# Optimization experiments

Hardware: AMD Instinct MI355X
Metric: run time of the kernel (lower is better)

The kernel has to match this reference:

```python
import jax, jax.numpy as jnp
import numpy as np

H = 512
L = 4096
LOC_CNT = 100000


def setup_inputs() -> dict:
    key = jax.random.key(0)
    ks = jax.random.split(key, 12)
    stdv = 1.0 / np.sqrt(H)

    def unif(k, shape):
        return jax.random.uniform(k, shape, dtype=jnp.float32, minval=-stdv, maxval=stdv)

    return {
        "td_upper": jax.random.uniform(ks[0], (L,), dtype=jnp.float32),
        "td_lower": jax.random.uniform(ks[1], (L,), dtype=jnp.float32),
        "ld_upper": jax.random.uniform(ks[2], (L,), dtype=jnp.float32),
        "ld_lower": jax.random.uniform(ks[3], (L,), dtype=jnp.float32),
        "loc": jax.random.randint(ks[4], (L,), 0, LOC_CNT, dtype=jnp.int64),
        "hx": jax.random.normal(ks[5], (H, 1), dtype=jnp.float32),
        "W_ih": unif(ks[6], (H, H)),
        "W_th_upper": unif(ks[7], (H, H)),
        "W_th_lower": unif(ks[8], (H, H)),
        "W_sh_upper": unif(ks[9], (H, H)),
        "W_sh_lower": unif(ks[10], (H, H)),
        "loc_table": unif(ks[11], (LOC_CNT, H)),
    }


def reference(td_upper, td_lower, ld_upper, ld_lower, loc, hx,
              W_ih, W_th_upper, W_th_lower, W_sh_upper, W_sh_lower, loc_table):
    # Gather location embeddings: (L, H)
    emb = loc_table[loc]
    # Ttd[i] @ emb[i] where Ttd[i] = (W_tu*tu_i + W_tl*tl_i)/(tu_i+tl_i):
    # distribute the scalar-weighted combine over the matmul.
    a = emb @ W_th_upper.T            # (L, H) == (W_th_upper @ emb[i])^T per row
    b = emb @ W_th_lower.T
    v = (a * td_upper[:, None] + b * td_lower[:, None]) / (td_upper + td_lower)[:, None]
    # Sld[i] @ v[i]
    c = v @ W_sh_upper.T
    d = v @ W_sh_lower.T
    w = (c * ld_upper[:, None] + d * ld_lower[:, None]) / (ld_upper + ld_lower)[:, None]
    # Original: torch.sum(torch.cat(...)) -> full scalar reduction over all L*H values.
    loc_vec = jnp.sum(w)
    usr_vec = W_ih @ hx               # (H, 1)
    return jax.nn.sigmoid(loc_vec + usr_vec)
```

## Files before the change

### kernel.cpp

```cpp
#include <hip/hip_runtime.h>
#include <math.h>

namespace {

constexpr int H = 512;
constexpr int L = 4096;
constexpr int REPG = 8;
constexpr int REPS = 4;

constexpr int WS_SU  = 0;
constexpr int WS_SL  = WS_SU + REPS * H;
constexpr int WS_G   = WS_SL + REPS * H;
constexpr int WS_IHV = WS_G + REPG * 4 * H;
constexpr int WS_ACC = WS_IHV + H;
constexpr int WS_CNT = WS_ACC + 1;
constexpr int WS_TOT = WS_CNT + 1;

constexpr int GB = 128;
constexpr int CB = 128;
constexpr int WB = 8;
constexpr int BGRID = 128;

__device__ inline float wave_reduce(float v) {
#pragma unroll
    for (int off = 32; off; off >>= 1) v += __shfl_xor(v, off, 64);
    return v;
}

__global__ __launch_bounds__(512) void stageA_k(
    const float* __restrict__ tu, const float* __restrict__ tl,
    const float* __restrict__ lu, const float* __restrict__ ll,
    const int* __restrict__ loc, const float* __restrict__ table,
    const float* __restrict__ Wsu, const float* __restrict__ Wsl,
    const float* __restrict__ Wih, const float* __restrict__ hx,
    float* __restrict__ ws) {
    const int b = blockIdx.x;
    const int t = threadIdx.x;
    if (b < GB) {
        const int rep = b & (REPG - 1);
        float aa = 0.f, ab = 0.f, ag = 0.f, ad = 0.f;
        const int row0 = b * (L / GB);
#pragma unroll 16
        for (int r = 0; r < L / GB; ++r) {
            const int row = row0 + r;
            const float tuv = tu[row], tlv = tl[row];
            const float luv = lu[row], llv = ll[row];
            const float ti = 1.f / (tuv + tlv), li = 1.f / (luv + llv);
            const float Tu = tuv * ti, Tl = tlv * ti;
            const float Lu = luv * li, Ll = llv * li;
            const float e = table[(size_t)loc[row] * H + t];
            aa += Lu * Tu * e;
            ab += Lu * Tl * e;
            ag += Ll * Tu * e;
            ad += Ll * Tl * e;
        }
        float* g = ws + WS_G + rep * (4 * H);
        atomicAdd(g + 0 * H + t, aa);
        atomicAdd(g + 1 * H + t, ab);
        atomicAdd(g + 2 * H + t, ag);
        atomicAdd(g + 3 * H + t, ad);
    } else if (b < GB + CB) {
        const int cb = b - GB;
        const int mat = cb >> 6;
        const int q = cb & 63;
        const int m0 = q * (H / 64);
        const int rep = q & (REPS - 1);
        const float* W = mat ? Wsl : Wsu;
        float acc = 0.f;
#pragma unroll
        for (int r = 0; r < H / 64; ++r) acc += W[(size_t)(m0 + r) * H + t];
        atomicAdd(ws + (mat ? WS_SL : WS_SU) + rep * H + t, acc);
    } else {
        const int wb = b - GB - CB;
        const int lane = t & 63, wid = t >> 6;
        const int j = lane * 8;
        const float4 xA = *reinterpret_cast<const float4*>(hx + j);
        const float4 xB = *reinterpret_cast<const float4*>(hx + j + 4);
#pragma unroll
        for (int r = 0; r < 8; ++r) {
            const int row = wb * 64 + wid * 8 + r;
            const float4 wA = *reinterpret_cast<const float4*>(Wih + (size_t)row * H + j);
            const float4 wB = *reinterpret_cast<const float4*>(Wih + (size_t)row * H + j + 4);
            float a = wA.x * xA.x + wA.y * xA.y + wA.z * xA.z + wA.w * xA.w
                    + wB.x * xB.x + wB.y * xB.y + wB.z * xB.z + wB.w * xB.w;
            a = wave_reduce(a);
            if (lane == 0) ws[WS_IHV + row] = a;
        }
    }
}

__global__ __launch_bounds__(512) void stageB_k(
    const float* __restrict__ Wtu, const float* __restrict__ Wtl,
    float* __restrict__ ws, float* __restrict__ out) {
    const int t = threadIdx.x;
    const int lane = t & 63, wid = t >> 6;
    const int gw = blockIdx.x * 8 + wid;
    const int mat = gw >> 9;
    const int h = gw & (H - 1);
    const float* W = mat ? Wtl : Wtu;
    const int v1 = mat ? 1 : 0;
    const int v2 = mat ? 3 : 2;

    float suh = 0.f, slh = 0.f;
#pragma unroll
    for (int rp = 0; rp < REPS; ++rp) {
        suh += ws[WS_SU + rp * H + h];
        slh += ws[WS_SL + rp * H + h];
    }

    const int j = lane * 8;
    float a1[8] = {0, 0, 0, 0, 0, 0, 0, 0};
    float a2[8] = {0, 0, 0, 0, 0, 0, 0, 0};
#pragma unroll
    for (int rp = 0; rp < REPG; ++rp) {
        const float* g1 = ws + WS_G + (rp * 4 + v1) * H + j;
        const float* g2 = ws + WS_G + (rp * 4 + v2) * H + j;
        const float4 x0 = *reinterpret_cast<const float4*>(g1);
        const float4 x1 = *reinterpret_cast<const float4*>(g1 + 4);
        const float4 y0 = *reinterpret_cast<const float4*>(g2);
        const float4 y1 = *reinterpret_cast<const float4*>(g2 + 4);
        a1[0] += x0.x; a1[1] += x0.y; a1[2] += x0.z; a1[3] += x0.w;
        a1[4] += x1.x; a1[5] += x1.y; a1[6] += x1.z; a1[7] += x1.w;
        a2[0] += y0.x; a2[1] += y0.y; a2[2] += y0.z; a2[3] += y0.w;
        a2[4] += y1.x; a2[5] += y1.y; a2[6] += y1.z; a2[7] += y1.w;
    }

    const float4 wA = *reinterpret_cast<const float4*>(W + (size_t)h * H + j);
    const float4 wB = *reinterpret_cast<const float4*>(W + (size_t)h * H + j + 4);
    float acc = wA.x * (suh * a1[0] + slh * a2[0])
              + wA.y * (suh * a1[1] + slh * a2[1])
              + wA.z * (suh * a1[2] + slh * a2[2])
              + wA.w * (suh * a1[3] + slh * a2[3])
              + wB.x * (suh * a1[4] + slh * a2[4])
              + wB.y * (suh * a1[5] + slh * a2[5])
              + wB.z * (suh * a1[6] + slh * a2[6])
              + wB.w * (suh * a1[7] + slh * a2[7]);
    acc = wave_reduce(acc);

    __shared__ float wp[8];
    __shared__ float accs;
    __shared__ int lastf;
    if (lane == 0) wp[wid] = acc;
    __syncthreads();
    if (t == 0) {
        float s = 0.f;
#pragma unroll
        for (int w = 0; w < 8; ++w) s += wp[w];
        atomicAdd(ws + WS_ACC, s);
        __threadfence();
        const int old = atomicAdd(reinterpret_cast<int*>(ws) + WS_CNT, 1);
        lastf = (old == (int)gridDim.x - 1) ? 1 : 0;
    }
    __syncthreads();
    if (lastf) {
        if (t == 0) accs = atomicAdd(ws + WS_ACC, 0.0f);
        __syncthreads();
        const float x = accs + ws[WS_IHV + t];
        out[t] = 1.f / (1.f + expf(-x));
    }
}

}

extern "C" void kernel_launch(void* const* d_in, const int* in_sizes, int n_in,
                              void* d_out, int out_size, void* d_ws, size_t ws_size,
                              hipStream_t stream) {
    const float* tu    = (const float*)d_in[0];
    const float* tl    = (const float*)d_in[1];
    const float* lu    = (const float*)d_in[2];
    const float* ll    = (const float*)d_in[3];
    const int*   loc   = (const int*)d_in[4];
    const float* hx    = (const float*)d_in[5];
    const float* Wih   = (const float*)d_in[6];
    const float* Wtu   = (const float*)d_in[7];
    const float* Wtl   = (const float*)d_in[8];
    const float* Wsu   = (const float*)d_in[9];
    const float* Wsl   = (const float*)d_in[10];
    const float* table = (const float*)d_in[11];
    float* ws  = (float*)d_ws;
    float* out = (float*)d_out;

    hipMemsetAsync(ws, 0, WS_TOT * sizeof(float), stream);
    stageA_k<<<GB + CB + WB, 512, 0, stream>>>(tu, tl, lu, ll, loc, table,
                                               Wsu, Wsl, Wih, hx, ws);
    stageB_k<<<BGRID, 512, 0, stream>>>(Wtu, Wtl, ws, out);
}
```

Baseline: 274.6 us.

## Fuse two stages into one kernel with a grid-wide done-counter barrier

Merges the gather/column-sum stage and the final matvec stage into a single launch. The final-stage blocks compute the column sums, prefetch their W_th rows, then spin on a global completion counter before reading the partial sums. This removes one kernel launch and the gap between launches, but relies on all 264 blocks being resident at once; a bounded spin loop guards against a hang.

```diff
diff --git a/kernel.cpp b/kernel.cpp
--- a/kernel.cpp
+++ b/kernel.cpp
@@ -8,18 +8,20 @@
 constexpr int REPG = 8;
 constexpr int REPS = 4;
 
-constexpr int WS_SU  = 0;
-constexpr int WS_SL  = WS_SU + REPS * H;
-constexpr int WS_G   = WS_SL + REPS * H;
-constexpr int WS_IHV = WS_G + REPG * 4 * H;
-constexpr int WS_ACC = WS_IHV + H;
-constexpr int WS_CNT = WS_ACC + 1;
-constexpr int WS_TOT = WS_CNT + 1;
-
-constexpr int GB = 128;
-constexpr int CB = 128;
-constexpr int WB = 8;
-constexpr int BGRID = 128;
+constexpr int WS_SU   = 0;
+constexpr int WS_SL   = WS_SU + REPS * H;
+constexpr int WS_G    = WS_SL + REPS * H;
+constexpr int WS_IHV  = WS_G + REPG * 4 * H;
+constexpr int WS_ACC  = WS_IHV + H;
+constexpr int WS_CNT  = WS_ACC + 1;
+constexpr int WS_DONE = WS_CNT + 1;
+constexpr int WS_TOT  = WS_DONE + 1;
+
+constexpr int NGATHER = 128;
+constexpr int NWIH    = 8;
+constexpr int NBLIN   = 128;
+constexpr int NGRID   = NGATHER + NWIH + NBLIN;
+constexpr int DONE_TARGET = NGATHER + NWIH + NBLIN;
 
 __device__ inline float wave_reduce(float v) {
 #pragma unroll
@@ -27,21 +29,32 @@
     return v;
 }
 
-__global__ __launch_bounds__(512) void stageA_k(
+__device__ inline void signal_done(int* done, int t) {
+    __syncthreads();
+    if (t == 0) {
+        __threadfence();
+        atomicAdd(done, 1);
+    }
+}
+
+__global__ __launch_bounds__(512) void fused_k(
     const float* __restrict__ tu, const float* __restrict__ tl,
     const float* __restrict__ lu, const float* __restrict__ ll,
     const int* __restrict__ loc, const float* __restrict__ table,
     const float* __restrict__ Wsu, const float* __restrict__ Wsl,
     const float* __restrict__ Wih, const float* __restrict__ hx,
-    float* __restrict__ ws) {
+    const float* __restrict__ Wtu, const float* __restrict__ Wtl,
+    float* __restrict__ ws, float* __restrict__ out) {
     const int b = blockIdx.x;
     const int t = threadIdx.x;
-    if (b < GB) {
+    int* const done = reinterpret_cast<int*>(ws) + WS_DONE;
+
+    if (b < NGATHER) {
         const int rep = b & (REPG - 1);
         float aa = 0.f, ab = 0.f, ag = 0.f, ad = 0.f;
-        const int row0 = b * (L / GB);
+        const int row0 = b * (L / NGATHER);
 #pragma unroll 16
-        for (int r = 0; r < L / GB; ++r) {
+        for (int r = 0; r < L / NGATHER; ++r) {
             const int row = row0 + r;
             const float tuv = tu[row], tlv = tl[row];
             const float luv = lu[row], llv = ll[row];
@@ -59,19 +72,9 @@
         atomicAdd(g + 1 * H + t, ab);
         atomicAdd(g + 2 * H + t, ag);
         atomicAdd(g + 3 * H + t, ad);
-    } else if (b < GB + CB) {
-        const int cb = b - GB;
-        const int mat = cb >> 6;
-        const int q = cb & 63;
-        const int m0 = q * (H / 64);
-        const int rep = q & (REPS - 1);
-        const float* W = mat ? Wsl : Wsu;
-        float acc = 0.f;
-#pragma unroll
-        for (int r = 0; r < H / 64; ++r) acc += W[(size_t)(m0 + r) * H + t];
-        atomicAdd(ws + (mat ? WS_SL : WS_SU) + rep * H + t, acc);
-    } else {
-        const int wb = b - GB - CB;
+        signal_done(done, t);
+    } else if (b < NGATHER + NWIH) {
+        const int wb = b - NGATHER;
         const int lane = t & 63, wid = t >> 6;
         const int j = lane * 8;
         const float4 xA = *reinterpret_cast<const float4*>(hx + j);
@@ -86,77 +89,96 @@
             a = wave_reduce(a);
             if (lane == 0) ws[WS_IHV + row] = a;
         }
-    }
-}
-
-__global__ __launch_bounds__(512) void stageB_k(
-    const float* __restrict__ Wtu, const float* __restrict__ Wtl,
-    float* __restrict__ ws, float* __restrict__ out) {
-    const int t = threadIdx.x;
-    const int lane = t & 63, wid = t >> 6;
-    const int gw = blockIdx.x * 8 + wid;
-    const int mat = gw >> 9;
-    const int h = gw & (H - 1);
-    const float* W = mat ? Wtl : Wtu;
-    const int v1 = mat ? 1 : 0;
-    const int v2 = mat ? 3 : 2;
-
-    float suh = 0.f, slh = 0.f;
-#pragma unroll
-    for (int rp = 0; rp < REPS; ++rp) {
-        suh += ws[WS_SU + rp * H + h];
-        slh += ws[WS_SL + rp * H + h];
-    }
-
-    const int j = lane * 8;
-    float a1[8] = {0, 0, 0, 0, 0, 0, 0, 0};
-    float a2[8] = {0, 0, 0, 0, 0, 0, 0, 0};
-#pragma unroll
-    for (int rp = 0; rp < REPG; ++rp) {
-        const float* g1 = ws + WS_G + (rp * 4 + v1) * H + j;
-        const float* g2 = ws + WS_G + (rp * 4 + v2) * H + j;
-        const float4 x0 = *reinterpret_cast<const float4*>(g1);
-        const float4 x1 = *reinterpret_cast<const float4*>(g1 + 4);
-        const float4 y0 = *reinterpret_cast<const float4*>(g2);
-        const float4 y1 = *reinterpret_cast<const float4*>(g2 + 4);
-        a1[0] += x0.x; a1[1] += x0.y; a1[2] += x0.z; a1[3] += x0.w;
-        a1[4] += x1.x; a1[5] += x1.y; a1[6] += x1.z; a1[7] += x1.w;
-        a2[0] += y0.x; a2[1] += y0.y; a2[2] += y0.z; a2[3] += y0.w;
-        a2[4] += y1.x; a2[5] += y1.y; a2[6] += y1.z; a2[7] += y1.w;
-    }
-
-    const float4 wA = *reinterpret_cast<const float4*>(W + (size_t)h * H + j);
-    const float4 wB = *reinterpret_cast<const float4*>(W + (size_t)h * H + j + 4);
-    float acc = wA.x * (suh * a1[0] + slh * a2[0])
-              + wA.y * (suh * a1[1] + slh * a2[1])
-              + wA.z * (suh * a1[2] + slh * a2[2])
-              + wA.w * (suh * a1[3] + slh * a2[3])
-              + wB.x * (suh * a1[4] + slh * a2[4])
-              + wB.y * (suh * a1[5] + slh * a2[5])
-              + wB.z * (suh * a1[6] + slh * a2[6])
-              + wB.w * (suh * a1[7] + slh * a2[7]);
-    acc = wave_reduce(acc);
-
-    __shared__ float wp[8];
-    __shared__ float accs;
-    __shared__ int lastf;
-    if (lane == 0) wp[wid] = acc;
-    __syncthreads();
-    if (t == 0) {
-        float s = 0.f;
-#pragma unroll
-        for (int w = 0; w < 8; ++w) s += wp[w];
-        atomicAdd(ws + WS_ACC, s);
+        signal_done(done, t);
+    } else {
+        const int cb = b - NGATHER - NWIH;
+        const int lane = t & 63, wid = t >> 6;
+
+        {
+            const int mat = cb >> 6;
+            const int q = cb & 63;
+            const int m0 = q * (H / 64);
+            const int rep = q & (REPS - 1);
+            const float* W = mat ? Wsl : Wsu;
+            float acc = 0.f;
+#pragma unroll
+            for (int r = 0; r < H / 64; ++r) acc += W[(size_t)(m0 + r) * H + t];
+            atomicAdd(ws + (mat ? WS_SL : WS_SU) + rep * H + t, acc);
+        }
+        signal_done(done, t);
+
+        const int gw = cb * 8 + wid;
+        const int mat = gw >> 9;
+        const int h = gw & (H - 1);
+        const float* W = mat ? Wtl : Wtu;
+        const int v1 = mat ? 1 : 0;
+        const int v2 = mat ? 3 : 2;
+        const int j = lane * 8;
+        const float4 wA = *reinterpret_cast<const float4*>(W + (size_t)h * H + j);
+        const float4 wB = *reinterpret_cast<const float4*>(W + (size_t)h * H + j + 4);
+
+        if (t == 0) {
+            int it = 0;
+            while (atomicAdd(done, 0) < DONE_TARGET && it < 10000000) {
+                ++it;
+                __builtin_amdgcn_s_sleep(8);
+            }
+        }
+        __syncthreads();
         __threadfence();
-        const int old = atomicAdd(reinterpret_cast<int*>(ws) + WS_CNT, 1);
-        lastf = (old == (int)gridDim.x - 1) ? 1 : 0;
-    }
-    __syncthreads();
-    if (lastf) {
-        if (t == 0) accs = atomicAdd(ws + WS_ACC, 0.0f);
+
+        float suh = 0.f, slh = 0.f;
+#pragma unroll
+        for (int rp = 0; rp < REPS; ++rp) {
+            suh += ws[WS_SU + rp * H + h];
+            slh += ws[WS_SL + rp * H + h];
+        }
+        float a1[8] = {0, 0, 0, 0, 0, 0, 0, 0};
+        float a2[8] = {0, 0, 0, 0, 0, 0, 0, 0};
+#pragma unroll
+        for (int rp = 0; rp < REPG; ++rp) {
+            const float* g1 = ws + WS_G + (rp * 4 + v1) * H + j;
+            const float* g2 = ws + WS_G + (rp * 4 + v2) * H + j;
+            const float4 x0 = *reinterpret_cast<const float4*>(g1);
+            const float4 x1 = *reinterpret_cast<const float4*>(g1 + 4);
+            const float4 y0 = *reinterpret_cast<const float4*>(g2);
+            const float4 y1 = *reinterpret_cast<const float4*>(g2 + 4);
+            a1[0] += x0.x; a1[1] += x0.y; a1[2] += x0.z; a1[3] += x0.w;
+            a1[4] += x1.x; a1[5] += x1.y; a1[6] += x1.z; a1[7] += x1.w;
+            a2[0] += y0.x; a2[1] += y0.y; a2[2] += y0.z; a2[3] += y0.w;
+            a2[4] += y1.x; a2[5] += y1.y; a2[6] += y1.z; a2[7] += y1.w;
+        }
+        float acc = wA.x * (suh * a1[0] + slh * a2[0])
+                  + wA.y * (suh * a1[1] + slh * a2[1])
+                  + wA.z * (suh * a1[2] + slh * a2[2])
+                  + wA.w * (suh * a1[3] + slh * a2[3])
+                  + wB.x * (suh * a1[4] + slh * a2[4])
+                  + wB.y * (suh * a1[5] + slh * a2[5])
+                  + wB.z * (suh * a1[6] + slh * a2[6])
+                  + wB.w * (suh * a1[7] + slh * a2[7]);
+        acc = wave_reduce(acc);
+
+        __shared__ float wp[8];
+        __shared__ float accs;
+        __shared__ int lastf;
+        if (lane == 0) wp[wid] = acc;
         __syncthreads();
-        const float x = accs + ws[WS_IHV + t];
-        out[t] = 1.f / (1.f + expf(-x));
+        if (t == 0) {
+            float s = 0.f;
+#pragma unroll
+            for (int w = 0; w < 8; ++w) s += wp[w];
+            atomicAdd(ws + WS_ACC, s);
+            __threadfence();
+            const int old = atomicAdd(reinterpret_cast<int*>(ws) + WS_CNT, 1);
+            lastf = (old == NBLIN - 1) ? 1 : 0;
+        }
+        __syncthreads();
+        if (lastf) {
+            if (t == 0) accs = atomicAdd(ws + WS_ACC, 0.0f);
+            __syncthreads();
+            const float x = accs + ws[WS_IHV + t];
+            out[t] = 1.f / (1.f + expf(-x));
+        }
     }
 }
 
@@ -181,7 +203,6 @@
     float* out = (float*)d_out;
 
     hipMemsetAsync(ws, 0, WS_TOT * sizeof(float), stream);
-    stageA_k<<<GB + CB + WB, 512, 0, stream>>>(tu, tl, lu, ll, loc, table,
-                                               Wsu, Wsl, Wih, hx, ws);
-    stageB_k<<<BGRID, 512, 0, stream>>>(Wtu, Wtl, ws, out);
-}
+    fused_k<<<NGRID, 512, 0, stream>>>(tu, tl, lu, ll, loc, table,
+                                       Wsu, Wsl, Wih, hx, Wtu, Wtl, ws, out);
+}
```

New measurement: 300.9 us. 9.6% more time.
